# Kernel tuning notes

Hardware: AMD Instinct MI355X
Metric: run time of the kernel (lower is better)

The kernel has to match this reference:

```python
import jax, jax.numpy as jnp
import numpy as np

B, T, C, L = 1024, 256, 128, 64
NEG = -1e30  # finite stand-in for -inf (safe gradients)
EPS = 1e-7   # keras.backend.epsilon()


def setup_inputs() -> dict:
    key = jax.random.key(0)
    k1, k2 = jax.random.split(key)
    # y_pred is a softmax output (probabilities), as keras ctc_batch_cost expects
    logits = jax.random.normal(k1, (B, T, C), dtype=jnp.float32)
    y_pred = jax.nn.softmax(logits, axis=-1)
    # labels in [0, C-2]; class C-1 is the CTC blank (keras convention)
    y_true = jax.random.randint(k2, (B, L), 0, C - 1, dtype=jnp.int64)
    return {"y_true": y_true, "y_pred": y_pred}


def ctc_loss(y_true, y_pred):
    """Negative log-likelihood CTC loss per sample, shape [B, 1].
    Matches keras.backend.ctc_batch_cost with full input/label lengths,
    blank index = num_classes - 1, log(y_pred + eps)."""
    Bb, Tt, Cc = y_pred.shape
    Ll = y_true.shape[1]
    blank = Cc - 1
    S = 2 * Ll + 1  # extended label: blank, l1, blank, l2, ..., blank

    logp = jnp.log(y_pred + EPS)  # [B, T, C]

    ext = jnp.full((Bb, S), blank, dtype=y_true.dtype).at[:, 1::2].set(y_true)  # [B, S]
    # per-(t, s) log-prob of the extended symbol: lp[b, t, s] = logp[b, t, ext[b, s]]
    lp = jnp.take_along_axis(logp, ext[:, None, :], axis=2)  # [B, T, S]

    # skip transition s-2 -> s allowed iff ext[s] != blank and ext[s] != ext[s-2]
    ext_m2 = jnp.concatenate(
        [jnp.full((Bb, 2), blank, dtype=ext.dtype), ext[:, :-2]], axis=1)
    can_skip = (ext != blank) & (ext != ext_m2)  # [B, S]

    def shift1(a):
        return jnp.concatenate(
            [jnp.full((Bb, 1), NEG, dtype=a.dtype), a[:, :-1]], axis=1)

    # alpha init at t=0: only s=0 (blank) and s=1 (first label) reachable
    alpha0 = (jnp.full((Bb, S), NEG, dtype=lp.dtype)
              .at[:, 0].set(lp[:, 0, 0])
              .at[:, 1].set(lp[:, 0, 1]))

    def step(alpha, lp_t):
        a1 = shift1(alpha)
        a2 = jnp.where(can_skip, shift1(shift1(alpha)), NEG)
        new = jax.nn.logsumexp(jnp.stack([alpha, a1, a2], axis=0), axis=0) + lp_t
        return new, None

    lp_tbs = jnp.swapaxes(lp, 0, 1)  # [T, B, S]
    alpha, _ = jax.lax.scan(step, alpha0, lp_tbs[1:])

    log_lik = jnp.logaddexp(alpha[:, S - 1], alpha[:, S - 2])  # end on last blank or last label
    return -log_lik[:, None]  # [B, 1], matching ctc_batch_cost output shape


def reference(y_true, y_pred):
    return ctc_loss(y_true, y_pred)
```

## Files before the change

kernel.cpp:

```cpp
#include <hip/hip_runtime.h>
#include <math.h>


#define Bn 1024
#define Tn 256
#define Cn 128
#define Ln 64
#define Sn 129
#define BLANK 127
#define NEGV (-1e30f)
#define EPSV (1e-7f)
#define CHUNK 8

__global__ __launch_bounds__(128)
void ctc_fwd_kernel(const int* __restrict__ y_true,
                    const float* __restrict__ y_pred,
                    float* __restrict__ out) {
    const int b   = blockIdx.x;
    const int tid = threadIdx.x;

    __shared__ __align__(16) float prob[2][CHUNK * Cn];
    __shared__ float alpha[2][Sn + 3];

    if (tid < 2) { alpha[0][tid] = NEGV; alpha[1][tid] = NEGV; }

    const int* lab = y_true + b * Ln;
    int  cls;
    bool canskip;
    if (tid & 1) {
        const int li = tid >> 1;
        const int lv = lab[li];
        cls = lv;
        canskip = (li == 0) ? true : (lv != lab[li - 1]);
    } else {
        cls = BLANK;
        canskip = false;
    }

    const float4* src = (const float4*)(y_pred + (size_t)b * (Tn * Cn));

    float4 p0 = src[tid];
    float4 p1 = src[tid + 128];

    int ab = 0;
    for (int c = 0; c < Tn / CHUNK; ++c) {
        const int pbuf = c & 1;
        ((float4*)prob[pbuf])[tid]       = p0;
        ((float4*)prob[pbuf])[tid + 128] = p1;
        if (c + 1 < Tn / CHUNK) {
            const float4* s2 = src + (c + 1) * (CHUNK * Cn / 4);
            p0 = s2[tid];
            p1 = s2[tid + 128];
        }
        __syncthreads();

        const float* pr = prob[pbuf];
        #pragma unroll
        for (int tt = 0; tt < CHUNK; ++tt) {
            if (c == 0 && tt == 0) {
                float* cur = alpha[ab];
                float v = NEGV;
                if (tid == 0)      v = __logf(pr[BLANK] + EPSV);
                else if (tid == 1) v = __logf(pr[cls]   + EPSV);
                cur[tid + 2] = v;
                if (tid == 127) cur[128 + 2] = NEGV;
                __syncthreads();
                continue;
            }
            const float* cur = alpha[ab];
            float*       nxt = alpha[ab ^ 1];
            const float* row = pr + tt * Cn;

            const float lp = __logf(row[cls] + EPSV);
            const float a0 = cur[tid + 2];
            const float a1 = cur[tid + 1];
            const float a2 = canskip ? cur[tid] : NEGV;
            const float m  = fmaxf(a0, fmaxf(a1, a2));
            const float r  = m + __logf(__expf(a0 - m) + __expf(a1 - m) + __expf(a2 - m)) + lp;

            float r128 = 0.0f;
            if (tid == 127) {
                const float b0 = cur[128 + 2];
                const float b1 = cur[127 + 2];
                const float lpb = __logf(row[BLANK] + EPSV);
                const float mm = fmaxf(b0, b1);
                r128 = mm + __logf(__expf(b0 - mm) + __expf(b1 - mm)) + lpb;
            }

            nxt[tid + 2] = r;
            if (tid == 127) nxt[128 + 2] = r128;
            ab ^= 1;
            __syncthreads();
        }
    }

    if (tid == 127) {
        const float* fin = alpha[ab];
        const float x = fin[128 + 2];
        const float y = fin[127 + 2];
        const float m = fmaxf(x, y);
        out[b] = -(m + __logf(__expf(x - m) + __expf(y - m)));
    }
}

extern "C" void kernel_launch(void* const* d_in, const int* in_sizes, int n_in,
                              void* d_out, int out_size, void* d_ws, size_t ws_size,
                              hipStream_t stream) {
    const int*   y_true = (const int*)d_in[0];
    const float* y_pred = (const float*)d_in[1];
    float*       out    = (float*)d_out;
    hipLaunchKernelGGL(ctc_fwd_kernel, dim3(Bn), dim3(128), 0, stream,
                       y_true, y_pred, out);
}
```

Before: 228.5 us.

## Run CTC alpha recursion in a single wavefront using register state and bpermute

Moves from 128 threads per sample with shared-memory alpha and a block barrier every timestep to a single 64-lane wavefront. Each lane holds one label's odd state and the following blank's even state in registers, and gets its neighbours through ds_bpermute, so the per-step __syncthreads goes away. Only the two needed probabilities per lane are gathered from global memory, with the next group of steps prefetched, instead of staging whole rows in LDS. All math moves to base-2 log/exp, with a final conversion back to natural log. The risk is that the strided scattered global gathers and the lower thread count per block may not hide latency as well as the coalesced row loads did.

```diff
diff --git a/kernel.cpp b/kernel.cpp
--- a/kernel.cpp
+++ b/kernel.cpp
@@ -6,100 +6,114 @@
 #define Tn 256
 #define Cn 128
 #define Ln 64
-#define Sn 129
 #define BLANK 127
-#define NEGV (-1e30f)
+#define NEG2 (-1.0e30f)
 #define EPSV (1e-7f)
-#define CHUNK 8
+#define U 8
+#define NG (Tn / U)
 
-__global__ __launch_bounds__(128)
-void ctc_fwd_kernel(const int* __restrict__ y_true,
-                    const float* __restrict__ y_pred,
-                    float* __restrict__ out) {
-    const int b   = blockIdx.x;
-    const int tid = threadIdx.x;
+#if __has_builtin(__builtin_amdgcn_exp2f)
+#define EXP2(x) __builtin_amdgcn_exp2f(x)
+#else
+#define EXP2(x) exp2f(x)
+#endif
+#if __has_builtin(__builtin_amdgcn_logf)
+#define LOG2(x) __builtin_amdgcn_logf(x)
+#else
+#define LOG2(x) log2f(x)
+#endif
 
-    __shared__ __align__(16) float prob[2][CHUNK * Cn];
-    __shared__ float alpha[2][Sn + 3];
-
-    if (tid < 2) { alpha[0][tid] = NEGV; alpha[1][tid] = NEGV; }
+__global__ __launch_bounds__(64)
+void ctc_wave_kernel(const int* __restrict__ y_true,
+                     const float* __restrict__ y_pred,
+                     float* __restrict__ out) {
+    const int b = blockIdx.x;
+    const int i = threadIdx.x;
 
     const int* lab = y_true + b * Ln;
-    int  cls;
-    bool canskip;
-    if (tid & 1) {
-        const int li = tid >> 1;
-        const int lv = lab[li];
-        cls = lv;
-        canskip = (li == 0) ? true : (lv != lab[li - 1]);
-    } else {
-        cls = BLANK;
-        canskip = false;
-    }
+    const int  li   = lab[i];
+    const int  lim1 = (i == 0) ? -1 : lab[i - 1];
+    const bool skip = (li != lim1);
 
-    const float4* src = (const float4*)(y_pred + (size_t)b * (Tn * Cn));
+    const float* base   = y_pred + (size_t)b * (Tn * Cn);
+    const float* pl_ptr = base + li;
+    const float* pb_ptr = base + BLANK;
 
-    float4 p0 = src[tid];
-    float4 p1 = src[tid + 128];
+    const int baddr = ((i - 1) & 63) << 2;
 
-    int ab = 0;
-    for (int c = 0; c < Tn / CHUNK; ++c) {
-        const int pbuf = c & 1;
-        ((float4*)prob[pbuf])[tid]       = p0;
-        ((float4*)prob[pbuf])[tid + 128] = p1;
-        if (c + 1 < Tn / CHUNK) {
-            const float4* s2 = src + (c + 1) * (CHUNK * Cn / 4);
-            p0 = s2[tid];
-            p1 = s2[tid + 128];
+    float lpl[2][U], lpb[2][U];
+    {
+        float rl[U], rb[U];
+        #pragma unroll
+        for (int j = 0; j < U; ++j) {
+            rl[j] = pl_ptr[j * Cn];
+            rb[j] = pb_ptr[j * Cn];
         }
-        __syncthreads();
-
-        const float* pr = prob[pbuf];
         #pragma unroll
-        for (int tt = 0; tt < CHUNK; ++tt) {
-            if (c == 0 && tt == 0) {
-                float* cur = alpha[ab];
-                float v = NEGV;
-                if (tid == 0)      v = __logf(pr[BLANK] + EPSV);
-                else if (tid == 1) v = __logf(pr[cls]   + EPSV);
-                cur[tid + 2] = v;
-                if (tid == 127) cur[128 + 2] = NEGV;
-                __syncthreads();
-                continue;
-            }
-            const float* cur = alpha[ab];
-            float*       nxt = alpha[ab ^ 1];
-            const float* row = pr + tt * Cn;
-
-            const float lp = __logf(row[cls] + EPSV);
-            const float a0 = cur[tid + 2];
-            const float a1 = cur[tid + 1];
-            const float a2 = canskip ? cur[tid] : NEGV;
-            const float m  = fmaxf(a0, fmaxf(a1, a2));
-            const float r  = m + __logf(__expf(a0 - m) + __expf(a1 - m) + __expf(a2 - m)) + lp;
-
-            float r128 = 0.0f;
-            if (tid == 127) {
-                const float b0 = cur[128 + 2];
-                const float b1 = cur[127 + 2];
-                const float lpb = __logf(row[BLANK] + EPSV);
-                const float mm = fmaxf(b0, b1);
-                r128 = mm + __logf(__expf(b0 - mm) + __expf(b1 - mm)) + lpb;
-            }
-
-            nxt[tid + 2] = r;
-            if (tid == 127) nxt[128 + 2] = r128;
-            ab ^= 1;
-            __syncthreads();
+        for (int j = 0; j < U; ++j) {
+            lpl[0][j] = LOG2(rl[j] + EPSV);
+            lpb[0][j] = LOG2(rb[j] + EPSV);
         }
     }
 
-    if (tid == 127) {
-        const float* fin = alpha[ab];
-        const float x = fin[128 + 2];
-        const float y = fin[127 + 2];
-        const float m = fmaxf(x, y);
-        out[b] = -(m + __logf(__expf(x - m) + __expf(y - m)));
+    float A0 = NEG2, Aod = NEG2, Aev = NEG2;
+
+    for (int g = 0; g < NG; ++g) {
+        const int cur = g & 1, nxt = cur ^ 1;
+        float rl[U], rb[U];
+        if (g + 1 < NG) {
+            const float* pl2 = pl_ptr + (size_t)(g + 1) * U * Cn;
+            const float* pb2 = pb_ptr + (size_t)(g + 1) * U * Cn;
+            #pragma unroll
+            for (int j = 0; j < U; ++j) {
+                rl[j] = pl2[j * Cn];
+                rb[j] = pb2[j * Cn];
+            }
+        }
+        #pragma unroll
+        for (int j = 0; j < U; ++j) {
+            const float lb = lpb[cur][j];
+            const float ll = lpl[cur][j];
+            if (g == 0 && j == 0) {
+                A0  = lb;
+                Aod = (i == 0) ? ll : NEG2;
+                Aev = NEG2;
+                continue;
+            }
+            const float odL_raw = __int_as_float(
+                __builtin_amdgcn_ds_bpermute(baddr, __float_as_int(Aod)));
+            const float evL_raw = __int_as_float(
+                __builtin_amdgcn_ds_bpermute(baddr, __float_as_int(Aev)));
+            const float evL = (i == 0) ? A0   : evL_raw;
+            const float odL = (i == 0) ? NEG2 : odL_raw;
+
+            const float m2  = fmaxf(Aev, Aod);
+            const float d2  = fminf(Aev, Aod) - m2;
+            const float nev = m2 + LOG2(1.0f + EXP2(d2)) + lb;
+
+            const float c3  = skip ? odL : NEG2;
+            const float m3  = fmaxf(fmaxf(Aod, evL), c3);
+            const float s3  = EXP2(Aod - m3) + EXP2(evL - m3) + EXP2(c3 - m3);
+            const float nod = m3 + LOG2(s3) + ll;
+
+            A0 += lb;
+            Aod = nod;
+            Aev = nev;
+        }
+        if (g + 1 < NG) {
+            #pragma unroll
+            for (int j = 0; j < U; ++j) {
+                lpl[nxt][j] = LOG2(rl[j] + EPSV);
+                lpb[nxt][j] = LOG2(rb[j] + EPSV);
+            }
+        }
+    }
+
+    if (i == 63) {
+        const float m = fmaxf(Aev, Aod);
+        const float d = fminf(Aev, Aod) - m;
+        const float ll2 = m + LOG2(1.0f + EXP2(d));
+        out[b] = -(ll2 * 0.69314718055994530942f);
     }
 }
 
@@ -109,6 +123,6 @@
     const int*   y_true = (const int*)d_in[0];
     const float* y_pred = (const float*)d_in[1];
     float*       out    = (float*)d_out;
-    hipLaunchKernelGGL(ctc_fwd_kernel, dim3(Bn), dim3(128), 0, stream,
+    hipLaunchKernelGGL(ctc_wave_kernel, dim3(Bn), dim3(64), 0, stream,
                        y_true, y_pred, out);
 }
```

Measured after the change: 197.6 us. 13.5% less time.
